# Performance work log

Measured on AMD Instinct MI355X. Metric: run time of the kernel, lower is better.

The kernel has to match this reference:

```python
import jax, jax.numpy as jnp
import numpy as np

B, Q, NCLS1, C = 8, 900, 11, 256
NUM_ANCHOR = 100
H, W = 200, 200


def _make_view(b):
    # maps homogeneous (x0, y0, x1, y1, 1) box coords (meters-ish) to BEV pixels:
    # pixel = 20 * coord + 100  (keeps random boxes inside the 200x200 grid)
    v = np.zeros((5, 5), dtype=np.float32)
    for i in range(4):
        v[i, i] = 20.0
        v[i, 4] = 100.0
    v[4, 4] = 1.0
    return jnp.asarray(np.broadcast_to(v, (b, 5, 5)).copy())


def setup_inputs() -> dict:
    key = jax.random.key(0)
    k1, k2, k3 = jax.random.split(key, 3)
    return {
        "pred_boxes": jax.random.normal(k1, (B, Q, 4), dtype=jnp.float32),
        "pred_logits": jax.random.normal(k2, (B, Q, NCLS1), dtype=jnp.float32),
        "box_feats": jax.random.normal(k3, (B, Q, C), dtype=jnp.float32),
        "view": _make_view(B),
    }


def _box_to_bev(pred_boxes, pred_logits, box_feats, view):
    # scores = max over non-background classes of softmax(logits)
    scores = jnp.max(jax.nn.softmax(pred_logits, axis=-1)[..., :-1], axis=-1)  # [b,Q]
    _, idx = jax.lax.top_k(scores, NUM_ANCHOR)                                 # [b,N]

    boxes = jnp.take_along_axis(pred_boxes, idx[:, :, None], axis=1)[..., :4]  # [b,N,4]
    feats = jnp.take_along_axis(box_feats, idx[:, :, None], axis=1)            # [b,N,C]

    cx, cy = boxes[..., 0], boxes[..., 1]
    w, h = jnp.exp(boxes[..., 2]), jnp.exp(boxes[..., 3])
    xyxy = jnp.stack([cx - 0.5 * w, cy - 0.5 * h, cx + 0.5 * w, cy + 0.5 * h], axis=-1)
    xyxy1 = jnp.concatenate([xyxy, jnp.ones_like(xyxy[..., :1])], axis=-1)     # [b,N,5]

    coords = jnp.einsum("bij,bnj->bni", view, xyxy1)[..., :4].astype(jnp.int32)
    x0 = jnp.clip(coords[..., 0], 0, W)
    y0 = jnp.clip(coords[..., 1], 0, H)
    x1 = jnp.clip(coords[..., 2], 0, W)
    y1 = jnp.clip(coords[..., 3], 0, H)

    ys = jnp.arange(H, dtype=jnp.int32)
    xs = jnp.arange(W, dtype=jnp.int32)
    row = (ys[None, None, :] >= y0[:, :, None]) & (ys[None, None, :] < y1[:, :, None])  # [b,N,H]
    col = (xs[None, None, :] >= x0[:, :, None]) & (xs[None, None, :] < x1[:, :, None])  # [b,N,W]
    region = row[:, :, :, None] & col[:, :, None, :]                                    # [b,N,H,W]

    bev = jnp.einsum("bnhw,bnc->bhwc", region.astype(feats.dtype), feats)  # [b,H,W,C]
    mask = jnp.any(region, axis=1)                                          # [b,H,W]
    return bev, mask


def reference(pred_boxes, pred_logits, box_feats, view):
    return _box_to_bev(pred_boxes, pred_logits, box_feats, view)
```

## Files before the change

kernel.cpp:

```cpp
#include <hip/hip_runtime.h>
#include <math.h>

#define B_    8
#define Q_    900
#define NCLS_ 11
#define NANC_ 100
#define H_    200
#define W_    200
#define C_    256

__global__ __launch_bounds__(1024) void segdet_topk_kernel(
    const float* __restrict__ pred_boxes,
    const float* __restrict__ pred_logits,
    const float* __restrict__ view,
    int*  __restrict__ ws_idx,
    int4* __restrict__ ws_box)
{
    const int b = blockIdx.x;
    const int q = threadIdx.x;

    __shared__ float sc[Q_];

    if (q < Q_) {
        const float* l = pred_logits + (b * Q_ + q) * NCLS_;
        float v[NCLS_];
        float m = -INFINITY;
        #pragma unroll
        for (int i = 0; i < NCLS_; ++i) { v[i] = l[i]; m = fmaxf(m, v[i]); }
        float s = 0.0f, e10 = -INFINITY;
        #pragma unroll
        for (int i = 0; i < NCLS_; ++i) {
            float e = expf(v[i] - m);
            s += e;
            if (i < NCLS_ - 1) e10 = fmaxf(e10, e);
        }
        sc[q] = e10 / s;
    }
    __syncthreads();

    if (q < Q_) {
        const float my = sc[q];
        int rank = 0;
        for (int j = 0; j < Q_; ++j) {
            float o = sc[j];
            rank += (o > my) || (o == my && j < q);
        }
        if (rank < NANC_) {
            const float* bx = pred_boxes + (b * Q_ + q) * 4;
            double cx = (double)bx[0], cy = (double)bx[1];
            double w  = exp((double)bx[2]);
            double h  = exp((double)bx[3]);
            double p[5] = { cx - 0.5 * w, cy - 0.5 * h,
                            cx + 0.5 * w, cy + 0.5 * h, 1.0 };
            const float* v5 = view + b * 25;
            int ico[4];
            #pragma unroll
            for (int i = 0; i < 4; ++i) {
                double acc = 0.0;
                #pragma unroll
                for (int j = 0; j < 5; ++j) acc += (double)v5[i * 5 + j] * p[j];
                ico[i] = (int)acc;
            }
            int x0 = min(max(ico[0], 0), W_);
            int y0 = min(max(ico[1], 0), H_);
            int x1 = min(max(ico[2], 0), W_);
            int y1 = min(max(ico[3], 0), H_);
            const int slot = b * NANC_ + rank;
            ws_idx[slot] = q;
            ws_box[slot] = make_int4(x0, y0, x1, y1);
        }
    }
}

__global__ __launch_bounds__(256) void segdet_bev_kernel(
    const float* __restrict__ box_feats,
    const int*   __restrict__ ws_idx,
    const int4*  __restrict__ ws_box,
    float* __restrict__ bev,
    float* __restrict__ mask)
{
    const int b   = blockIdx.x / H_;
    const int h   = blockIdx.x % H_;
    const int tid = threadIdx.x;
    const int ln  = tid & 63;
    const int wv  = tid >> 6;

    __shared__ int s_box[NANC_];
    __shared__ int s_nact;
    __shared__ int s_nopen[W_];
    __shared__ int s_scan[256];
    __shared__ int s_ofs[W_ + 1];
    __shared__ int s_evpos[W_];
    __shared__ int s_ent[2 * NANC_];
    __shared__ int s_wtot[4];
    __shared__ int s_nev;

    if (tid < 64) {
        int na = 0;
        #pragma unroll
        for (int it = 0; it < 2; ++it) {
            int k = it * 64 + ln;
            bool act = false;
            int packed = 0;
            if (k < NANC_) {
                int4 bx = ws_box[b * NANC_ + k];
                int qi  = ws_idx[b * NANC_ + k];
                act = (bx.y <= h) && (h < bx.w) && (bx.x < bx.z);
                packed = bx.x | (bx.z << 8) | (qi << 16);
            }
            unsigned long long ball = __ballot(act);
            int pos = na + (int)__popcll(ball & ((1ull << ln) - 1ull));
            if (act) s_box[pos] = packed;
            na += (int)__popcll(ball);
        }
        if (ln == 0) s_nact = na;
    }
    __syncthreads();

    const int nact = s_nact;

    int ntot = 0;
    if (tid < W_) {
        int nopen = 0, nclose = 0, cov = 0;
        for (int k = 0; k < nact; ++k) {
            int pk = s_box[k];
            int x0 = pk & 0xFF, x1 = (pk >> 8) & 0xFF;
            nopen  += (x0 == tid);
            nclose += (x1 == tid);
            cov    += (x0 <= tid) && (tid < x1);
        }
        s_nopen[tid] = nopen;
        ntot = nopen + nclose;
        mask[(size_t)(b * H_ + h) * W_ + tid] = (cov > 0) ? 1.0f : 0.0f;
    }
    s_scan[tid] = ntot;
    __syncthreads();

    #pragma unroll
    for (int d = 1; d < 256; d <<= 1) {
        int v = s_scan[tid];
        int u = (tid >= d) ? s_scan[tid - d] : 0;
        __syncthreads();
        s_scan[tid] = v + u;
        __syncthreads();
    }
    if (tid < W_) s_ofs[tid] = s_scan[tid] - ntot;
    if (tid == 0) s_ofs[W_] = s_scan[255];

    bool flag = (tid < W_) && (ntot > 0);
    unsigned long long bal = __ballot(flag);
    if (ln == 0) s_wtot[wv] = (int)__popcll(bal);
    __syncthreads();
    int off = 0;
    for (int i = 0; i < wv; ++i) off += s_wtot[i];
    if (flag) s_evpos[off + (int)__popcll(bal & ((1ull << ln) - 1ull))] = tid;
    if (tid == 0) s_nev = s_wtot[0] + s_wtot[1] + s_wtot[2] + s_wtot[3];

    if (tid < nact) {
        int pk = s_box[tid];
        int x0 = pk & 0xFF, x1 = (pk >> 8) & 0xFF, q = pk >> 16;
        int ro = 0, rc = 0;
        for (int j = 0; j < tid; ++j) {
            int pj = s_box[j];
            ro += ((pj & 0xFF) == x0);
            rc += (((pj >> 8) & 0xFF) == x1);
        }
        s_ent[s_ofs[x0] + ro] = q;
        if (x1 < W_) s_ent[s_ofs[x1] + s_nopen[x1] + rc] = q | (1 << 31);
    }
    __syncthreads();

    const int nev = s_nev;
    const float* fbase = box_feats + (size_t)b * Q_ * C_ + ln * 4;
    float* obase = bev + (size_t)(b * H_ + h) * W_ * C_ + ln * 4;

    float4 acc = make_float4(0.f, 0.f, 0.f, 0.f);
    int cnt = 0;
    int p = 0;
    int nextpix = (0 < nev) ? s_evpos[0] : W_;
    for (int w = wv; w < W_; w += 4) {
        while (w >= nextpix) {
            int e1 = s_ofs[nextpix + 1];
            for (int e = s_ofs[nextpix]; e < e1; ++e) {
                int ent = s_ent[e];
                int q = ent & 0xFFFF;
                const float4 f = *(const float4*)(fbase + (size_t)q * C_);
                if (ent < 0) { acc.x -= f.x; acc.y -= f.y; acc.z -= f.z; acc.w -= f.w; --cnt; }
                else         { acc.x += f.x; acc.y += f.y; acc.z += f.z; acc.w += f.w; ++cnt; }
            }
            ++p;
            nextpix = (p < nev) ? s_evpos[p] : W_;
        }
        if (cnt == 0) acc = make_float4(0.f, 0.f, 0.f, 0.f);
        *(float4*)(obase + (size_t)w * C_) = acc;
    }
}

extern "C" void kernel_launch(void* const* d_in, const int* in_sizes, int n_in,
                              void* d_out, int out_size, void* d_ws, size_t ws_size,
                              hipStream_t stream) {
    const float* pred_boxes  = (const float*)d_in[0];
    const float* pred_logits = (const float*)d_in[1];
    const float* box_feats   = (const float*)d_in[2];
    const float* view        = (const float*)d_in[3];

    float* bev  = (float*)d_out;
    float* mask = bev + (size_t)B_ * H_ * W_ * C_;

    int*  ws_idx = (int*)d_ws;
    int4* ws_box = (int4*)((char*)d_ws + 3200);

    segdet_topk_kernel<<<B_, 1024, 0, stream>>>(pred_boxes, pred_logits, view,
                                                ws_idx, ws_box);
    segdet_bev_kernel<<<B_ * H_, 256, 0, stream>>>(box_feats, ws_idx, ws_box,
                                                   bev, mask);
}
```

Before: 112.0 us.

## Give each wave a contiguous column segment and scan with wave shuffles

Each of the four waves now handles a contiguous quarter of the row's columns instead of every fourth column. A wave first seeds its accumulator by summing the features of boxes that cover its starting column, then sweeps only the open/close events inside its own segment, writing runs of identical output pixels between events. This removes the redundant full-row event traversal each wave used to do. The shared-memory Hillis-Steele scan with many barriers is replaced by a wave-level shuffle scan plus a small cross-wave sum, and the event-position compaction is dropped. The cost is an extra pass over active boxes per wave to compute the seed coverage.

```diff
diff --git a/kernel.cpp b/kernel.cpp
--- a/kernel.cpp
+++ b/kernel.cpp
@@ -8,6 +8,7 @@
 #define H_    200
 #define W_    200
 #define C_    256
+#define QTR_  (W_ / 4)
 
 __global__ __launch_bounds__(1024) void segdet_topk_kernel(
     const float* __restrict__ pred_boxes,
@@ -88,12 +89,9 @@
     __shared__ int s_box[NANC_];
     __shared__ int s_nact;
     __shared__ int s_nopen[W_];
-    __shared__ int s_scan[256];
-    __shared__ int s_ofs[W_ + 1];
-    __shared__ int s_evpos[W_];
+    __shared__ int s_ofs[W_];
     __shared__ int s_ent[2 * NANC_];
-    __shared__ int s_wtot[4];
-    __shared__ int s_nev;
+    __shared__ int s_wsum[4];
 
     if (tid < 64) {
         int na = 0;
@@ -133,28 +131,21 @@
         ntot = nopen + nclose;
         mask[(size_t)(b * H_ + h) * W_ + tid] = (cov > 0) ? 1.0f : 0.0f;
     }
-    s_scan[tid] = ntot;
-    __syncthreads();
-
+
+    int incl = ntot;
     #pragma unroll
-    for (int d = 1; d < 256; d <<= 1) {
-        int v = s_scan[tid];
-        int u = (tid >= d) ? s_scan[tid - d] : 0;
-        __syncthreads();
-        s_scan[tid] = v + u;
-        __syncthreads();
-    }
-    if (tid < W_) s_ofs[tid] = s_scan[tid] - ntot;
-    if (tid == 0) s_ofs[W_] = s_scan[255];
-
-    bool flag = (tid < W_) && (ntot > 0);
-    unsigned long long bal = __ballot(flag);
-    if (ln == 0) s_wtot[wv] = (int)__popcll(bal);
-    __syncthreads();
-    int off = 0;
-    for (int i = 0; i < wv; ++i) off += s_wtot[i];
-    if (flag) s_evpos[off + (int)__popcll(bal & ((1ull << ln) - 1ull))] = tid;
-    if (tid == 0) s_nev = s_wtot[0] + s_wtot[1] + s_wtot[2] + s_wtot[3];
+    for (int d = 1; d < 64; d <<= 1) {
+        int u = __shfl_up(incl, d);
+        incl = (ln >= d) ? incl + u : incl;
+    }
+    if (ln == 63) s_wsum[wv] = incl;
+    __syncthreads();
+    int prev = 0;
+    #pragma unroll
+    for (int j = 0; j < 4; ++j) prev += (j < wv) ? s_wsum[j] : 0;
+    const int ne = s_wsum[0] + s_wsum[1] + s_wsum[2] + s_wsum[3];
+    if (tid < W_) s_ofs[tid] = prev + incl - ntot;
+    __syncthreads();
 
     if (tid < nact) {
         int pk = s_box[tid];
@@ -165,35 +156,50 @@
             ro += ((pj & 0xFF) == x0);
             rc += (((pj >> 8) & 0xFF) == x1);
         }
-        s_ent[s_ofs[x0] + ro] = q;
-        if (x1 < W_) s_ent[s_ofs[x1] + s_nopen[x1] + rc] = q | (1 << 31);
-    }
-    __syncthreads();
-
-    const int nev = s_nev;
+        s_ent[s_ofs[x0] + ro] = x0 | (q << 8);
+        if (x1 < W_)
+            s_ent[s_ofs[x1] + s_nopen[x1] + rc] = x1 | (q << 8) | (1 << 31);
+    }
+    __syncthreads();
+
+    const int start = wv * QTR_;
+    const int end   = start + QTR_;
+
     const float* fbase = box_feats + (size_t)b * Q_ * C_ + ln * 4;
     float* obase = bev + (size_t)(b * H_ + h) * W_ * C_ + ln * 4;
 
     float4 acc = make_float4(0.f, 0.f, 0.f, 0.f);
     int cnt = 0;
-    int p = 0;
-    int nextpix = (0 < nev) ? s_evpos[0] : W_;
-    for (int w = wv; w < W_; w += 4) {
-        while (w >= nextpix) {
-            int e1 = s_ofs[nextpix + 1];
-            for (int e = s_ofs[nextpix]; e < e1; ++e) {
-                int ent = s_ent[e];
-                int q = ent & 0xFFFF;
-                const float4 f = *(const float4*)(fbase + (size_t)q * C_);
-                if (ent < 0) { acc.x -= f.x; acc.y -= f.y; acc.z -= f.z; acc.w -= f.w; --cnt; }
-                else         { acc.x += f.x; acc.y += f.y; acc.z += f.z; acc.w += f.w; ++cnt; }
-            }
-            ++p;
-            nextpix = (p < nev) ? s_evpos[p] : W_;
-        }
+    for (int k = 0; k < nact; ++k) {
+        int pk = s_box[k];
+        int x0 = pk & 0xFF, x1 = (pk >> 8) & 0xFF;
+        if (x0 <= start && start < x1) {
+            const float4 f = *(const float4*)(fbase + (size_t)(pk >> 16) * C_);
+            acc.x += f.x; acc.y += f.y; acc.z += f.z; acc.w += f.w;
+            ++cnt;
+        }
+    }
+
+    int e    = s_ofs[start + 1];
+    int eend = (end < W_) ? s_ofs[end] : ne;
+    int w    = start;
+    int entc = (e < eend) ? s_ent[e] : 0;
+    while (e < eend) {
+        int entn = (e + 1 < eend) ? s_ent[e + 1] : 0;
+        const int epix = entc & 0xFF;
+        const float4 f = *(const float4*)(fbase +
+                           (size_t)((entc >> 8) & 0x3FF) * C_);
         if (cnt == 0) acc = make_float4(0.f, 0.f, 0.f, 0.f);
+        for (; w < epix; ++w)
+            *(float4*)(obase + (size_t)w * C_) = acc;
+        if (entc < 0) { acc.x -= f.x; acc.y -= f.y; acc.z -= f.z; acc.w -= f.w; --cnt; }
+        else          { acc.x += f.x; acc.y += f.y; acc.z += f.z; acc.w += f.w; ++cnt; }
+        entc = entn;
+        ++e;
+    }
+    if (cnt == 0) acc = make_float4(0.f, 0.f, 0.f, 0.f);
+    for (; w < end; ++w)
         *(float4*)(obase + (size_t)w * C_) = acc;
-    }
 }
 
 extern "C" void kernel_launch(void* const* d_in, const int* in_sizes, int n_in,
```

New measurement: 152.3 us. 35.9% more time.

## Split BEV row sweep into two column halves, reorder blocks, early-exit empty rows

Applied to the files above, without the earlier changes.

Each wave now sweeps only half of the row's columns, stepping by 2, instead of the full row stepping by 4. The upper-half waves start from an accumulator seeded with every active box that covers the middle column, and jump to the matching event index. This shortens the serial event-processing chain per wave. Blocks are also reordered so the batch index varies fastest and rows go outward from the centre, and rows with no active boxes just write zeros and exit early. The cost is extra feature loads to seed the upper half, plus more complex event-index bookkeeping.

```diff
diff --git a/kernel.cpp b/kernel.cpp
--- a/kernel.cpp
+++ b/kernel.cpp
@@ -8,6 +8,7 @@
 #define H_    200
 #define W_    200
 #define C_    256
+#define HHALF 100
 
 __global__ __launch_bounds__(1024) void segdet_topk_kernel(
     const float* __restrict__ pred_boxes,
@@ -79,8 +80,10 @@
     float* __restrict__ bev,
     float* __restrict__ mask)
 {
-    const int b   = blockIdx.x / H_;
-    const int h   = blockIdx.x % H_;
+    const int hidx = blockIdx.x / B_;
+    const int b    = blockIdx.x % B_;
+    const int h    = (hidx & 1) ? (HHALF - 1 - (hidx >> 1)) : (HHALF + (hidx >> 1));
+
     const int tid = threadIdx.x;
     const int ln  = tid & 63;
     const int wv  = tid >> 6;
@@ -93,6 +96,7 @@
     __shared__ int s_evpos[W_];
     __shared__ int s_ent[2 * NANC_];
     __shared__ int s_wtot[4];
+    __shared__ int s_plow;
     __shared__ int s_nev;
 
     if (tid < 64) {
@@ -118,6 +122,16 @@
     __syncthreads();
 
     const int nact = s_nact;
+    float* obase = bev + (size_t)(b * H_ + h) * W_ * C_ + ln * 4;
+    float* mrow  = mask + (size_t)(b * H_ + h) * W_;
+
+    if (nact == 0) {
+        const float4 z = make_float4(0.f, 0.f, 0.f, 0.f);
+        for (int w = wv; w < W_; w += 4)
+            *(float4*)(obase + (size_t)w * C_) = z;
+        if (tid < W_) mrow[tid] = 0.0f;
+        return;
+    }
 
     int ntot = 0;
     if (tid < W_) {
@@ -131,7 +145,7 @@
         }
         s_nopen[tid] = nopen;
         ntot = nopen + nclose;
-        mask[(size_t)(b * H_ + h) * W_ + tid] = (cov > 0) ? 1.0f : 0.0f;
+        mrow[tid] = (cov > 0) ? 1.0f : 0.0f;
     }
     s_scan[tid] = ntot;
     __syncthreads();
@@ -150,6 +164,8 @@
     bool flag = (tid < W_) && (ntot > 0);
     unsigned long long bal = __ballot(flag);
     if (ln == 0) s_wtot[wv] = (int)__popcll(bal);
+    if (wv == 1 && ln == 0)
+        s_plow = (int)__popcll(bal & ((1ull << 37) - 1ull));
     __syncthreads();
     int off = 0;
     for (int i = 0; i < wv; ++i) off += s_wtot[i];
@@ -171,14 +187,29 @@
     __syncthreads();
 
     const int nev = s_nev;
+    const bool upper = (wv >= 2);
+    const int  wbeg  = upper ? (HHALF + (wv - 2)) : wv;
+    const int  wlim  = upper ? W_ : HHALF;
+    const int  p_lo  = s_wtot[0] + s_plow;
+
     const float* fbase = box_feats + (size_t)b * Q_ * C_ + ln * 4;
-    float* obase = bev + (size_t)(b * H_ + h) * W_ * C_ + ln * 4;
 
     float4 acc = make_float4(0.f, 0.f, 0.f, 0.f);
     int cnt = 0;
-    int p = 0;
-    int nextpix = (0 < nev) ? s_evpos[0] : W_;
-    for (int w = wv; w < W_; w += 4) {
+    if (upper) {
+        for (int k = 0; k < nact; ++k) {
+            int pk = s_box[k];
+            int x0 = pk & 0xFF, x1 = (pk >> 8) & 0xFF;
+            if (x0 <= HHALF && HHALF < x1) {
+                const float4 f = *(const float4*)(fbase + (size_t)(pk >> 16) * C_);
+                acc.x += f.x; acc.y += f.y; acc.z += f.z; acc.w += f.w;
+                ++cnt;
+            }
+        }
+    }
+    int p = upper ? p_lo : 0;
+    int nextpix = (p < nev) ? s_evpos[p] : W_;
+    for (int w = wbeg; w < wlim; w += 2) {
         while (w >= nextpix) {
             int e1 = s_ofs[nextpix + 1];
             for (int e = s_ofs[nextpix]; e < e1; ++e) {
```

Result: no change. 114.2 us (+2.0%).
